# Optimization experiments

Measured on AMD Instinct MI355X. Metric: run time of the kernel, lower is better.

## Reference

```python
import jax, jax.numpy as jnp
import numpy as np

LN_EPS = 1e-3  # Keras LayerNormalization default epsilon
MASK_PENALTY = 1.0e9  # Keras Attention masked-score penalty


def setup_inputs() -> dict:
    key = jax.random.key(0)
    k1, k2, k3, k4 = jax.random.split(key, 4)
    B, L, K, Gt, Gc, D = 4, 512, 512, 512, 256, 64
    return {
        "x": jax.random.normal(k1, (B, L, Gt), dtype=jnp.float32),
        "x_query": jax.random.normal(k2, (B, L, Gt, D), dtype=jnp.float32),
        "context_key": jax.random.normal(k3, (B, K, Gc, D), dtype=jnp.float32),
        "context_value": jax.random.normal(k4, (B, K, Gt), dtype=jnp.float32),
        "gamma": jnp.ones((Gt,), dtype=jnp.float32),
        "beta": jnp.zeros((Gt,), dtype=jnp.float32),
    }


def reference(x, x_query, context_key, context_value, gamma, beta):
    # scores[b,l,k] = sum_{m,p,n} q[b,l,m,n] * k[b,k,p,n]
    # einsum 'blmn,bkpn->blk' factorizes: reduce gene axes first, then contract
    # over the feature axis (algebraically identical, avoids a huge 5-D temp).
    q_red = x_query.sum(axis=2)        # [B, L, D]
    k_red = context_key.sum(axis=2)    # [B, K, D]
    scores = jnp.einsum("bld,bkd->blk", q_red, k_red)  # [B, L, K]

    # causal (lower-triangular) mask over [L, K]
    L, K = scores.shape[1], scores.shape[2]
    causal = jnp.tril(jnp.ones((L, K), dtype=bool))
    scores = scores - MASK_PENALTY * (~causal).astype(scores.dtype)

    weights = jax.nn.softmax(scores, axis=-1)                 # [B, L, K]
    attn_out = jnp.einsum("blk,bkg->blg", weights, context_value)  # [B, L, Gt]

    # residual add + LayerNorm over last axis
    y = x + attn_out
    mean = y.mean(axis=-1, keepdims=True)
    var = y.var(axis=-1, keepdims=True)
    out = (y - mean) * jax.lax.rsqrt(var + LN_EPS) * gamma + beta
    return out
```

## Files before the change

kernel.cpp:

```cpp
#include <hip/hip_runtime.h>

#define BB 4
#define LL 512
#define KK 512
#define GT 512
#define GC 256
#define DD 64

typedef float vf4 __attribute__((ext_vector_type(4)));

__global__ __launch_bounds__(256) void reduce_qk(const float* __restrict__ xq,
                                                 const float* __restrict__ ck,
                                                 float* __restrict__ qred,
                                                 float* __restrict__ kredT) {
    const int bid = blockIdx.x;
    const int tid = threadIdx.x;
    const int d4 = tid & 15;
    const int g = tid >> 4;

    const vf4* p;
    int iters;
    if (bid < BB * LL) {
        p = (const vf4*)(xq + (size_t)bid * GT * DD);
        iters = GT / 16;
    } else {
        const int bk = bid - BB * LL;
        p = (const vf4*)(ck + (size_t)bk * GC * DD);
        iters = GC / 16;
    }
    p += g * 16 + d4;

    vf4 acc = {0.f, 0.f, 0.f, 0.f};
    #pragma unroll 16
    for (int it = 0; it < iters; ++it) {
        vf4 v = __builtin_nontemporal_load(p);
        p += 256;
        acc += v;
    }

    __shared__ float s[16][64];
    s[g][d4 * 4 + 0] = acc.x;
    s[g][d4 * 4 + 1] = acc.y;
    s[g][d4 * 4 + 2] = acc.z;
    s[g][d4 * 4 + 3] = acc.w;
    __syncthreads();
    if (tid < 64) {
        float sum = 0.f;
        #pragma unroll
        for (int i = 0; i < 16; ++i) sum += s[i][tid];
        if (bid < BB * LL) {
            qred[(size_t)bid * DD + tid] = sum;
        } else {
            const int bk = bid - BB * LL;
            const int b = bk >> 9;
            const int k = bk & (KK - 1);
            kredT[(size_t)b * (16 * KK * 4) + (size_t)(tid >> 2) * (KK * 4)
                  + k * 4 + (tid & 3)] = sum;
        }
    }
}

__global__ __launch_bounds__(256) void attn_fused(
    const float* __restrict__ x, const float* __restrict__ qred,
    const float* __restrict__ kredT, const float* __restrict__ cv,
    const float* __restrict__ gamma, const float* __restrict__ beta,
    float* __restrict__ out) {
    const int bl = blockIdx.x;
    const int b = bl >> 9;
    const int l = bl & (LL - 1);
    const int tid = threadIdx.x;
    const int wv = tid >> 6;

    __shared__ float w[KK];
    __shared__ unsigned long long smask[8];
    __shared__ float redm[4], reds[4], red1[4], red2[4];

    const vf4* q4 = (const vf4*)(qred + (size_t)bl * DD);
    vf4 q[16];
    #pragma unroll
    for (int d = 0; d < 16; ++d) q[d] = q4[d];

    const float* ktb = kredT + (size_t)b * (16 * KK * 4);
    float sc[2];
    #pragma unroll
    for (int i = 0; i < 2; ++i) {
        const int k = tid + i * 256;
        float s = -1e30f;
        if (k <= l) {
            float acc = 0.f;
            #pragma unroll
            for (int dc = 0; dc < 16; ++dc) {
                vf4 kv = *(const vf4*)(ktb + (size_t)dc * (KK * 4) + k * 4);
                acc += kv.x * q[dc].x + kv.y * q[dc].y + kv.z * q[dc].z + kv.w * q[dc].w;
            }
            s = acc;
        }
        sc[i] = s;
    }

    float m = fmaxf(sc[0], sc[1]);
    #pragma unroll
    for (int off = 1; off < 64; off <<= 1) m = fmaxf(m, __shfl_xor(m, off));
    if ((tid & 63) == 0) redm[wv] = m;
    __syncthreads();
    m = fmaxf(fmaxf(redm[0], redm[1]), fmaxf(redm[2], redm[3]));

    const float e0 = expf(sc[0] - m);
    const float e1 = expf(sc[1] - m);
    float ssum = e0 + e1;
    #pragma unroll
    for (int off = 1; off < 64; off <<= 1) ssum += __shfl_xor(ssum, off);
    if ((tid & 63) == 0) reds[wv] = ssum;

    const unsigned long long b0 = __ballot(e0 > 0.f);
    const unsigned long long b1 = __ballot(e1 > 0.f);
    if ((tid & 63) == 0) { smask[wv] = b0; smask[wv + 4] = b1; }
    __syncthreads();
    ssum = reds[0] + reds[1] + reds[2] + reds[3];
    const float inv = 1.f / ssum;
    w[tid]       = e0 * inv;
    w[tid + 256] = e1 * inv;
    __syncthreads();

    const float2* cvb = (const float2*)(cv + (size_t)b * KK * GT);
    float2 acc = {0.f, 0.f};
    const int nwords = (l >> 6) + 1;
    for (int wd = 0; wd < nwords; ++wd) {
        unsigned long long msk = smask[wd];
        while (msk) {
            const int k = (wd << 6) + __builtin_ctzll(msk);
            msk &= msk - 1;
            const float wk = w[k];
            const float2 v = cvb[(size_t)k * (GT / 2) + tid];
            acc.x += wk * v.x;
            acc.y += wk * v.y;
        }
    }

    const float2 xv = ((const float2*)(x + (size_t)bl * GT))[tid];
    float2 y = {xv.x + acc.x, xv.y + acc.y};

    float s1 = y.x + y.y;
    float s2 = y.x * y.x + y.y * y.y;
    #pragma unroll
    for (int off = 1; off < 64; off <<= 1) {
        s1 += __shfl_xor(s1, off);
        s2 += __shfl_xor(s2, off);
    }
    if ((tid & 63) == 0) { red1[wv] = s1; red2[wv] = s2; }
    __syncthreads();
    s1 = red1[0] + red1[1] + red1[2] + red1[3];
    s2 = red2[0] + red2[1] + red2[2] + red2[3];

    const float mean = s1 * (1.f / GT);
    const float var = s2 * (1.f / GT) - mean * mean;
    const float rstd = rsqrtf(var + 1e-3f);

    const float2 ga = ((const float2*)gamma)[tid];
    const float2 be = ((const float2*)beta)[tid];
    float2 o;
    o.x = (y.x - mean) * rstd * ga.x + be.x;
    o.y = (y.y - mean) * rstd * ga.y + be.y;
    ((float2*)out)[(size_t)bl * (GT / 2) + tid] = o;
}

extern "C" void kernel_launch(void* const* d_in, const int* in_sizes, int n_in,
                              void* d_out, int out_size, void* d_ws, size_t ws_size,
                              hipStream_t stream) {
    const float* x     = (const float*)d_in[0];
    const float* xq    = (const float*)d_in[1];
    const float* ck    = (const float*)d_in[2];
    const float* cv    = (const float*)d_in[3];
    const float* gamma = (const float*)d_in[4];
    const float* beta  = (const float*)d_in[5];
    float* out = (float*)d_out;

    float* qred  = (float*)d_ws;
    float* kredT = qred + (size_t)BB * LL * DD;

    reduce_qk<<<BB * LL + BB * KK, 256, 0, stream>>>(xq, ck, qred, kredT);
    attn_fused<<<BB * LL, 256, 0, stream>>>(x, qred, kredT, cv, gamma, beta, out);
}
```

Measured before the change: 77.69 us.

## Map one query row per wavefront in fused attention kernel

Changes the attention kernel so each 64-lane wavefront handles a whole query row instead of each 256-thread block handling one row. Softmax max/sum and LayerNorm reductions become wave-level shuffles, removing the shared memory and all __syncthreads barriers. Weights are broadcast with __shfl, and context values, x and out are moved with 16-byte vector accesses. The cost is more registers per thread and a serial loop over up to 512 keys inside each wave, with causal rows giving different waves in a block very different work.

```diff
diff --git a/kernel.cpp b/kernel.cpp
--- a/kernel.cpp
+++ b/kernel.cpp
@@ -65,15 +65,13 @@
     const float* __restrict__ kredT, const float* __restrict__ cv,
     const float* __restrict__ gamma, const float* __restrict__ beta,
     float* __restrict__ out) {
-    const int bl = blockIdx.x;
-    const int b = bl >> 9;
-    const int l = bl & (LL - 1);
+    const int bid = blockIdx.x;
     const int tid = threadIdx.x;
     const int wv = tid >> 6;
-
-    __shared__ float w[KK];
-    __shared__ unsigned long long smask[8];
-    __shared__ float redm[4], reds[4], red1[4], red2[4];
+    const int lane = tid & 63;
+    const int b = bid >> 7;
+    const int l = ((bid & 127) << 2) + wv;
+    const int bl = (b << 9) + l;
 
     const vf4* q4 = (const vf4*)(qred + (size_t)bl * DD);
     vf4 q[16];
@@ -81,11 +79,12 @@
     for (int d = 0; d < 16; ++d) q[d] = q4[d];
 
     const float* ktb = kredT + (size_t)b * (16 * KK * 4);
-    float sc[2];
+    const int jmax = l >> 6;
+    float sc[8];
     #pragma unroll
-    for (int i = 0; i < 2; ++i) {
-        const int k = tid + i * 256;
-        float s = -1e30f;
+    for (int j = 0; j < 8; ++j) sc[j] = -1e30f;
+    for (int j = 0; j <= jmax; ++j) {
+        const int k = (j << 6) + lane;
         if (k <= l) {
             float acc = 0.f;
             #pragma unroll
@@ -93,75 +92,68 @@
                 vf4 kv = *(const vf4*)(ktb + (size_t)dc * (KK * 4) + k * 4);
                 acc += kv.x * q[dc].x + kv.y * q[dc].y + kv.z * q[dc].z + kv.w * q[dc].w;
             }
-            s = acc;
-        }
-        sc[i] = s;
-    }
-
-    float m = fmaxf(sc[0], sc[1]);
-    #pragma unroll
-    for (int off = 1; off < 64; off <<= 1) m = fmaxf(m, __shfl_xor(m, off));
-    if ((tid & 63) == 0) redm[wv] = m;
-    __syncthreads();
-    m = fmaxf(fmaxf(redm[0], redm[1]), fmaxf(redm[2], redm[3]));
-
-    const float e0 = expf(sc[0] - m);
-    const float e1 = expf(sc[1] - m);
-    float ssum = e0 + e1;
-    #pragma unroll
-    for (int off = 1; off < 64; off <<= 1) ssum += __shfl_xor(ssum, off);
-    if ((tid & 63) == 0) reds[wv] = ssum;
-
-    const unsigned long long b0 = __ballot(e0 > 0.f);
-    const unsigned long long b1 = __ballot(e1 > 0.f);
-    if ((tid & 63) == 0) { smask[wv] = b0; smask[wv + 4] = b1; }
-    __syncthreads();
-    ssum = reds[0] + reds[1] + reds[2] + reds[3];
-    const float inv = 1.f / ssum;
-    w[tid]       = e0 * inv;
-    w[tid + 256] = e1 * inv;
-    __syncthreads();
-
-    const float2* cvb = (const float2*)(cv + (size_t)b * KK * GT);
-    float2 acc = {0.f, 0.f};
-    const int nwords = (l >> 6) + 1;
-    for (int wd = 0; wd < nwords; ++wd) {
-        unsigned long long msk = smask[wd];
-        while (msk) {
-            const int k = (wd << 6) + __builtin_ctzll(msk);
-            msk &= msk - 1;
-            const float wk = w[k];
-            const float2 v = cvb[(size_t)k * (GT / 2) + tid];
-            acc.x += wk * v.x;
-            acc.y += wk * v.y;
+            sc[j] = acc;
         }
     }
 
-    const float2 xv = ((const float2*)(x + (size_t)bl * GT))[tid];
-    float2 y = {xv.x + acc.x, xv.y + acc.y};
+    float mx = sc[0];
+    #pragma unroll
+    for (int j = 1; j < 8; ++j) mx = fmaxf(mx, sc[j]);
+    #pragma unroll
+    for (int off = 1; off < 64; off <<= 1) mx = fmaxf(mx, __shfl_xor(mx, off));
 
-    float s1 = y.x + y.y;
-    float s2 = y.x * y.x + y.y * y.y;
+    float e[8];
+    float ssum = 0.f;
+    #pragma unroll
+    for (int j = 0; j < 8; ++j) { e[j] = expf(sc[j] - mx); ssum += e[j]; }
+    #pragma unroll
+    for (int off = 1; off < 64; off <<= 1) ssum += __shfl_xor(ssum, off);
+    const float inv = 1.f / ssum;
+    float w[8];
+    #pragma unroll
+    for (int j = 0; j < 8; ++j) w[j] = e[j] * inv;
+
+    const float* cvb = cv + (size_t)b * KK * GT;
+    vf4 a0 = {0.f, 0.f, 0.f, 0.f};
+    vf4 a1 = {0.f, 0.f, 0.f, 0.f};
+    for (int j = 0; j <= jmax; ++j) {
+        unsigned long long msk = __ballot(e[j] > 0.f);
+        while (msk) {
+            const int s = __builtin_ctzll(msk);
+            msk &= msk - 1;
+            const float wk = __shfl(w[j], s);
+            const int k = (j << 6) + s;
+            const vf4* vp = (const vf4*)(cvb + (size_t)k * GT) + lane * 2;
+            a0 += wk * vp[0];
+            a1 += wk * vp[1];
+        }
+    }
+
+    const vf4* x4 = (const vf4*)(x + (size_t)bl * GT) + lane * 2;
+    vf4 y0 = x4[0] + a0;
+    vf4 y1 = x4[1] + a1;
+
+    float s1 = y0.x + y0.y + y0.z + y0.w + y1.x + y1.y + y1.z + y1.w;
+    float s2 = y0.x * y0.x + y0.y * y0.y + y0.z * y0.z + y0.w * y0.w
+             + y1.x * y1.x + y1.y * y1.y + y1.z * y1.z + y1.w * y1.w;
     #pragma unroll
     for (int off = 1; off < 64; off <<= 1) {
         s1 += __shfl_xor(s1, off);
         s2 += __shfl_xor(s2, off);
     }
-    if ((tid & 63) == 0) { red1[wv] = s1; red2[wv] = s2; }
-    __syncthreads();
-    s1 = red1[0] + red1[1] + red1[2] + red1[3];
-    s2 = red2[0] + red2[1] + red2[2] + red2[3];
 
     const float mean = s1 * (1.f / GT);
     const float var = s2 * (1.f / GT) - mean * mean;
     const float rstd = rsqrtf(var + 1e-3f);
 
-    const float2 ga = ((const float2*)gamma)[tid];
-    const float2 be = ((const float2*)beta)[tid];
-    float2 o;
-    o.x = (y.x - mean) * rstd * ga.x + be.x;
-    o.y = (y.y - mean) * rstd * ga.y + be.y;
-    ((float2*)out)[(size_t)bl * (GT / 2) + tid] = o;
+    const vf4* g4 = (const vf4*)gamma + lane * 2;
+    const vf4* be4 = (const vf4*)beta + lane * 2;
+    vf4 o0 = (y0 - mean) * rstd * g4[0] + be4[0];
+    vf4 o1 = (y1 - mean) * rstd * g4[1] + be4[1];
+
+    vf4* out4 = (vf4*)(out + (size_t)bl * GT) + lane * 2;
+    out4[0] = o0;
+    out4[1] = o1;
 }
 
 extern "C" void kernel_launch(void* const* d_in, const int* in_sizes, int n_in,
@@ -179,5 +171,5 @@
     float* kredT = qred + (size_t)BB * LL * DD;
 
     reduce_qk<<<BB * LL + BB * KK, 256, 0, stream>>>(xq, ck, qred, kredT);
-    attn_fused<<<BB * LL, 256, 0, stream>>>(x, qred, kredT, cv, gamma, beta, out);
+    attn_fused<<<BB * LL / 4, 256, 0, stream>>>(x, qred, kredT, cv, gamma, beta, out);
 }
```

Result: slower. 92.00 us (+18.4%).
